# Kernel tuning notes

Hardware: AMD Instinct MI355X
Metric: run time of the kernel (lower is better)

## Reference

```python
import jax, jax.numpy as jnp
import numpy as np

N = 100000
E = 1600000
H = 128
G = 64  # num graphs


def setup_inputs() -> dict:
    key = jax.random.key(0)
    ks = jax.random.split(key, 20)
    s = 1.0 / np.sqrt(H)
    inp = {
        'x': jax.random.normal(ks[0], (N,), jnp.float32),
        'edge_index': jax.random.randint(ks[1], (2, E), 0, N, jnp.int32),
        'edge_attr': jax.random.normal(ks[2], (E, 1), jnp.float32),
        'batch': jnp.sort(jax.random.randint(ks[3], (N,), 0, G, jnp.int32)),
        # node/edge encoders (Linear(1, H))
        'ne_w': jax.random.normal(ks[4], (1, H), jnp.float32),
        'ne_b': jnp.zeros((H,), jnp.float32),
        'ee_w': jax.random.normal(ks[5], (1, H), jnp.float32),
        'ee_b': jnp.zeros((H,), jnp.float32),
        # conv1: internal edge lin (Linear(H,H)) + MLP (H->H->H)
        'lin1_w': jax.random.normal(ks[6], (H, H), jnp.float32) * s,
        'lin1_b': jnp.zeros((H,), jnp.float32),
        'w11': jax.random.normal(ks[7], (H, H), jnp.float32) * s,
        'b11': jnp.zeros((H,), jnp.float32),
        'w12': jax.random.normal(ks[8], (H, H), jnp.float32) * s,
        'b12': jnp.zeros((H,), jnp.float32),
        # conv2
        'lin2_w': jax.random.normal(ks[9], (H, H), jnp.float32) * s,
        'lin2_b': jnp.zeros((H,), jnp.float32),
        'w21': jax.random.normal(ks[10], (H, H), jnp.float32) * s,
        'b21': jnp.zeros((H,), jnp.float32),
        'w22': jax.random.normal(ks[11], (H, H), jnp.float32) * s,
        'b22': jnp.zeros((H,), jnp.float32),
    }
    return inp


def _gine(h, edge_index, e, lin_w, lin_b, w1, b1, w2, b2, eps=0.0):
    # message: ReLU(x_j + Lin(edge_attr)), aggregated (sum) at target nodes
    src, dst = edge_index[0], edge_index[1]
    m = jax.nn.relu(h[src] + e @ lin_w + lin_b)           # [E, H]
    agg = jax.ops.segment_sum(m, dst, num_segments=N)      # [N, H]
    z = (1.0 + eps) * h + agg
    return jax.nn.relu(z @ w1 + b1) @ w2 + b2


def reference(x, edge_index, edge_attr, batch, ne_w, ne_b, ee_w, ee_b,
              lin1_w, lin1_b, w11, b11, w12, b12,
              lin2_w, lin2_b, w21, b21, w22, b22):
    h = x.reshape(-1, 1) @ ne_w + ne_b                     # [N, H]
    e = edge_attr @ ee_w + ee_b                            # [E, H]
    h = jax.nn.relu(_gine(h, edge_index, e, lin1_w, lin1_b, w11, b11, w12, b12))
    h = jax.nn.relu(_gine(h, edge_index, e, lin2_w, lin2_b, w21, b21, w22, b22))
    # global mean pool per graph
    sums = jax.ops.segment_sum(h, batch, num_segments=G)   # [G, H]
    cnt = jax.ops.segment_sum(jnp.ones((N,), h.dtype), batch, num_segments=G)
    return sums / jnp.maximum(cnt, 1.0)[:, None]
```

## Files before the change

kernel.cpp:

```cpp
#include <hip/hip_runtime.h>

typedef unsigned short u16;
typedef unsigned int u32;
typedef __bf16 bfrag __attribute__((ext_vector_type(8)));
typedef float f32x4 __attribute__((ext_vector_type(4)));
typedef float f32x2 __attribute__((ext_vector_type(2)));

__device__ __forceinline__ u16 f2bf(float f) {
    u32 u = __float_as_uint(f);
    u32 r = (u + 0x7FFFu + ((u >> 16) & 1u)) >> 16;
    return (u16)r;
}
__device__ __forceinline__ float bf2f(u32 h) {
    return __uint_as_float(h << 16);
}

__global__ __launch_bounds__(1024) void prepack_bcount_kernel(
    const int* __restrict__ dst, int* __restrict__ bcnt, int* __restrict__ done,
    int* __restrict__ bstart, int* __restrict__ bcur, int E, int nb, int nbc,
    const float* __restrict__ w11, const float* __restrict__ w12,
    const float* __restrict__ w21, const float* __restrict__ w22,
    u16* __restrict__ hi, u16* __restrict__ lo,
    const float* __restrict__ ne_b, const float* __restrict__ ee_w, const float* __restrict__ ee_b,
    const float* __restrict__ lin1_w, const float* __restrict__ lin1_b,
    const float* __restrict__ lin2_w, const float* __restrict__ lin2_b,
    float* __restrict__ u1, float* __restrict__ C1, float* __restrict__ u2, float* __restrict__ C2)
{
    if (blockIdx.x >= (u32)nbc) {
        int pb = blockIdx.x - nbc;
        if (pb == 64) {
            int c = threadIdx.x;
            if (c < 128) {
                float s1 = 0.f, t1 = 0.f, s2 = 0.f, t2 = 0.f;
                for (int k = 0; k < 128; ++k) {
                    float w1 = lin1_w[k * 128 + c];
                    float w2 = lin2_w[k * 128 + c];
                    float ew = ee_w[k], eb = ee_b[k];
                    s1 = fmaf(ew, w1, s1); t1 = fmaf(eb, w1, t1);
                    s2 = fmaf(ew, w2, s2); t2 = fmaf(eb, w2, t2);
                }
                u1[c] = s1; C1[c] = t1 + lin1_b[c] + ne_b[c];
                u2[c] = s2; C2[c] = t2 + lin2_b[c];
            }
            return;
        }
        int which = pb >> 4;
        const float* w = (which == 0) ? w11 : (which == 1) ? w12 : (which == 2) ? w21 : w22;
        int o = (pb & 15) * 1024 + threadIdx.x;
        int j = o & 7;
        int lane = (o >> 3) & 63;
        int ct = (o >> 9) & 7;
        int ks = o >> 12;
        int k = ks * 32 + ((lane >> 4) * 8) + j;
        int c = ct * 16 + (lane & 15);
        float v = w[k * 128 + c];
        u16 h = f2bf(v);
        float vh = bf2f(h);
        u16 l = f2bf(v - vh);
        hi[which * 16384 + o] = h;
        lo[which * 16384 + o] = l;
        return;
    }

    __shared__ int h[256];
    __shared__ int is_last;
    if (threadIdx.x < 256) h[threadIdx.x] = 0;
    __syncthreads();
    int idx = blockIdx.x * 1024 + threadIdx.x;
    int e = idx * 4;
    if (e + 3 < E) {
        int4 d4 = ((const int4*)dst)[idx];
        atomicAdd(&h[d4.x >> 9], 1);
        atomicAdd(&h[d4.y >> 9], 1);
        atomicAdd(&h[d4.z >> 9], 1);
        atomicAdd(&h[d4.w >> 9], 1);
    } else {
        for (int k = e; k < E; ++k) atomicAdd(&h[dst[k] >> 9], 1);
    }
    __syncthreads();
    if (threadIdx.x < 256 && h[threadIdx.x]) atomicAdd(&bcnt[threadIdx.x], h[threadIdx.x]);
    __syncthreads();
    if (threadIdx.x == 0) {
        __threadfence();
        is_last = (atomicAdd(done, 1) == nbc - 1);
    }
    __syncthreads();
    if (!is_last) return;
    if (threadIdx.x < 256) h[threadIdx.x] = atomicAdd(&bcnt[threadIdx.x], 0);
    __syncthreads();
    __shared__ int excl[256];
    if (threadIdx.x < 64) {
        int l = threadIdx.x;
        int v0 = h[4 * l], v1 = h[4 * l + 1], v2 = h[4 * l + 2], v3 = h[4 * l + 3];
        int tot = v0 + v1 + v2 + v3;
        int run = tot;
#pragma unroll
        for (int off = 1; off < 64; off <<= 1) {
            int t = __shfl_up(run, off);
            if (l >= off) run += t;
        }
        int ex = run - tot;
        excl[4 * l] = ex;
        excl[4 * l + 1] = ex + v0;
        excl[4 * l + 2] = ex + v0 + v1;
        excl[4 * l + 3] = ex + v0 + v1 + v2;
    }
    __syncthreads();
    if (threadIdx.x < nb) {
        int ex = excl[threadIdx.x];
        bstart[threadIdx.x] = ex;
        bcur[threadIdx.x] = ex;
        if (threadIdx.x == nb - 1) bstart[nb] = ex + h[threadIdx.x];
    }
}

__global__ __launch_bounds__(1024) void bin_kernel(
    const int* __restrict__ src, const int* __restrict__ dst, const float* __restrict__ eattr,
    int* __restrict__ bucket_cursor,
    int2* __restrict__ binned, int E, int nb)
{
    __shared__ int hist[256];
    __shared__ int basel[256];
    __shared__ int gbase[256];
    __shared__ int2 stage[4096];
    __shared__ unsigned char sb[4096];
    const int tid = threadIdx.x;
    const int e0 = blockIdx.x * 4096;
    const int valid = min(4096, E - e0);

    if (tid < 256) hist[tid] = 0;
    __syncthreads();

    int d[4], s[4], a[4], rk[4];
    bool ok[4];
    const int eb = e0 + tid * 4;
    if (eb + 3 < E) {
        int4 d4 = *(const int4*)(dst + eb);
        int4 s4 = *(const int4*)(src + eb);
        int4 a4 = *(const int4*)((const int*)eattr + eb);
        d[0] = d4.x; d[1] = d4.y; d[2] = d4.z; d[3] = d4.w;
        s[0] = s4.x; s[1] = s4.y; s[2] = s4.z; s[3] = s4.w;
        a[0] = a4.x; a[1] = a4.y; a[2] = a4.z; a[3] = a4.w;
        ok[0] = ok[1] = ok[2] = ok[3] = true;
    } else {
#pragma unroll
        for (int k = 0; k < 4; ++k) {
            int e = eb + k;
            ok[k] = e < E;
            if (ok[k]) {
                d[k] = dst[e];
                s[k] = src[e];
                a[k] = __float_as_int(eattr[e]);
            }
        }
    }
#pragma unroll
    for (int k = 0; k < 4; ++k) {
        if (ok[k]) rk[k] = atomicAdd(&hist[d[k] >> 9], 1);
    }
    __syncthreads();
    if (tid < 64) {
        int l = tid;
        int v0 = hist[4 * l], v1 = hist[4 * l + 1], v2 = hist[4 * l + 2], v3 = hist[4 * l + 3];
        int tot = v0 + v1 + v2 + v3;
        int run = tot;
#pragma unroll
        for (int off = 1; off < 64; off <<= 1) {
            int t = __shfl_up(run, off);
            if (l >= off) run += t;
        }
        int ex = run - tot;
        basel[4 * l] = ex;
        basel[4 * l + 1] = ex + v0;
        basel[4 * l + 2] = ex + v0 + v1;
        basel[4 * l + 3] = ex + v0 + v1 + v2;
    }
    __syncthreads();
    if (tid < nb && hist[tid] > 0) gbase[tid] = atomicAdd(&bucket_cursor[tid], hist[tid]);
#pragma unroll
    for (int k = 0; k < 4; ++k) {
        if (ok[k]) {
            int b = d[k] >> 9;
            int pos = basel[b] + rk[k];
            stage[pos] = make_int2(s[k] | ((d[k] & 511) << 17), a[k]);
            sb[pos] = (unsigned char)b;
        }
    }
    __syncthreads();
    for (int i = tid; i < valid; i += 1024) {
        int b = (int)sb[i];
        binned[gbase[b] + (i - basel[b])] = stage[i];
    }
}

__global__ __launch_bounds__(1024) void fine_kernel(
    const int2* __restrict__ binned, const int* __restrict__ bstart,
    int* __restrict__ rowptr, int2* __restrict__ edges, int N, int nbuckets)
{
    __shared__ int hist[512];
    __shared__ int excl[512];
    const int tid = threadIdx.x;
    const int b = blockIdx.x;
    const int s0 = bstart[b], s1 = bstart[b + 1];
    if (tid < 512) hist[tid] = 0;
    __syncthreads();
    for (int i = s0 + tid; i < s1; i += 1024)
        atomicAdd(&hist[(binned[i].x >> 17) & 511], 1);
    __syncthreads();
    if (tid < 64) {
        int l = tid;
        int v[8], pre[8];
        int tot = 0;
#pragma unroll
        for (int k = 0; k < 8; ++k) { v[k] = hist[8 * l + k]; pre[k] = tot; tot += v[k]; }
        int run = tot;
#pragma unroll
        for (int off = 1; off < 64; off <<= 1) {
            int t = __shfl_up(run, off);
            if (l >= off) run += t;
        }
        int ex = run - tot;
#pragma unroll
        for (int k = 0; k < 8; ++k) excl[8 * l + k] = ex + pre[k];
    }
    __syncthreads();
    const int nbase = b << 9;
    if (tid < 512 && nbase + tid < N) rowptr[nbase + tid] = s0 + excl[tid];
    if (b == nbuckets - 1 && tid == 0) rowptr[N] = s1;
    __syncthreads();
    for (int i = s0 + tid; i < s1; i += 1024) {
        int2 ed = binned[i];
        int dlo = (ed.x >> 17) & 511;
        ed.x &= 0x1FFFF;
        int pos = atomicAdd(&excl[dlo], 1);
        edges[s0 + pos] = ed;
    }
}


__global__ __launch_bounds__(256) void pull1_kernel(
    const float* __restrict__ x,
    const int* __restrict__ rowptr, const int2* __restrict__ edges,
    const float* __restrict__ ne_w, const float* __restrict__ ne_b,
    const float* __restrict__ u1, const float* __restrict__ C1,
    u16* __restrict__ zb, int N)
{
    int lane = threadIdx.x & 63;
    int node = blockIdx.x * 4 + (threadIdx.x >> 6);
    if (node >= N) return;
    f32x2 A  = *(const f32x2*)(ne_w + 2 * lane);
    f32x2 Bv = *(const f32x2*)(u1   + 2 * lane);
    f32x2 Cv = *(const f32x2*)(C1   + 2 * lane);
    f32x2 nb = *(const f32x2*)(ne_b + 2 * lane);
    const f32x2 zero = {0.f, 0.f};
    int jb = rowptr[node], je = rowptr[node + 1];
    f32x2 acc = zero;
    int j = jb;
    for (; j + 8 <= je; j += 8) {
        float xs[8], av[8];
#pragma unroll
        for (int t = 0; t < 8; ++t) {
            int2 ep = edges[j + t];
            int s = __builtin_amdgcn_readfirstlane(ep.x);
            av[t] = __int_as_float(__builtin_amdgcn_readfirstlane(ep.y));
            xs[t] = x[s];
        }
#pragma unroll
        for (int t = 0; t < 8; ++t) {
            f32x2 m = __builtin_elementwise_fma((f32x2){xs[t], xs[t]}, A,
                        __builtin_elementwise_fma((f32x2){av[t], av[t]}, Bv, Cv));
            acc += __builtin_elementwise_max(m, zero);
        }
    }
    for (; j < je; ++j) {
        int2 ep = edges[j];
        int s = __builtin_amdgcn_readfirstlane(ep.x);
        float av = __int_as_float(__builtin_amdgcn_readfirstlane(ep.y));
        float xs = x[s];
        f32x2 m = __builtin_elementwise_fma((f32x2){xs, xs}, A,
                    __builtin_elementwise_fma((f32x2){av, av}, Bv, Cv));
        acc += __builtin_elementwise_max(m, zero);
    }
    float xn = x[node];
    f32x2 z = __builtin_elementwise_fma((f32x2){xn, xn}, A, nb) + acc;
    ((u32*)(zb + (long)node * 128))[lane] = (u32)f2bf(z.x) | ((u32)f2bf(z.y) << 16);
}

__global__ __launch_bounds__(256) void pull2_kernel(
    const u16* __restrict__ h1b,
    const int* __restrict__ rowptr, const int2* __restrict__ edges,
    const float* __restrict__ u2, const float* __restrict__ C2,
    u16* __restrict__ zb2, int N)
{
    int lane = threadIdx.x & 63;
    int node = blockIdx.x * 4 + (threadIdx.x >> 6);
    if (node >= N) return;
    f32x2 Bv = *(const f32x2*)(u2 + 2 * lane);
    f32x2 Cv = *(const f32x2*)(C2 + 2 * lane);
    const f32x2 zero = {0.f, 0.f};
    int jb = rowptr[node], je = rowptr[node + 1];
    f32x2 acc = zero;
    int j = jb;
    for (; j + 8 <= je; j += 8) {
        int sidx[8];
        float av[8];
        u32 hv[8];
#pragma unroll
        for (int t = 0; t < 8; ++t) {
            int2 ep = edges[j + t];
            sidx[t] = __builtin_amdgcn_readfirstlane(ep.x);
            av[t] = __int_as_float(__builtin_amdgcn_readfirstlane(ep.y));
        }
#pragma unroll
        for (int t = 0; t < 8; ++t)
            hv[t] = *(const u32*)(h1b + (long)sidx[t] * 128 + 2 * lane);
#pragma unroll
        for (int t = 0; t < 8; ++t) {
            f32x2 h = { __uint_as_float(hv[t] << 16), __uint_as_float(hv[t] & 0xFFFF0000u) };
            f32x2 m = h + __builtin_elementwise_fma((f32x2){av[t], av[t]}, Bv, Cv);
            acc += __builtin_elementwise_max(m, zero);
        }
    }
    for (; j < je; ++j) {
        int2 ep = edges[j];
        int s = __builtin_amdgcn_readfirstlane(ep.x);
        float av = __int_as_float(__builtin_amdgcn_readfirstlane(ep.y));
        u32 hv = *(const u32*)(h1b + (long)s * 128 + 2 * lane);
        f32x2 h = { __uint_as_float(hv << 16), __uint_as_float(hv & 0xFFFF0000u) };
        f32x2 m = h + __builtin_elementwise_fma((f32x2){av, av}, Bv, Cv);
        acc += __builtin_elementwise_max(m, zero);
    }
    u32 hn = *(const u32*)(h1b + (long)node * 128 + 2 * lane);
    f32x2 hnv = { __uint_as_float(hn << 16), __uint_as_float(hn & 0xFFFF0000u) };
    f32x2 z = hnv + acc;
    ((u32*)(zb2 + (long)node * 128))[lane] = (u32)f2bf(z.x) | ((u32)f2bf(z.y) << 16);
}

__global__ __launch_bounds__(256) void mlp_kernel(
    const u16* __restrict__ zb,
    const u16* __restrict__ w1hi, const u16* __restrict__ w1lo,
    const u16* __restrict__ w2hi, const u16* __restrict__ w2lo,
    const float* __restrict__ b1, const float* __restrict__ b2,
    u16* __restrict__ outb)
{
    __shared__ __align__(16) u16 tls[64][136];
    const int lane = threadIdx.x & 63;
    const int wv = threadIdx.x >> 6;
    const int m = lane & 15;
    const int q = lane >> 4;
    const int ko = q * 8;
    const long tile_row = (long)blockIdx.x * 64 + wv * 16;

    f32x4 acc[8];
#pragma unroll
    for (int ct = 0; ct < 8; ++ct) acc[ct] = (f32x4){0.f, 0.f, 0.f, 0.f};

#pragma unroll
    for (int ks = 0; ks < 4; ++ks) {
        bfrag a = *(const bfrag*)(zb + (tile_row + m) * 128 + ks * 32 + ko);
#pragma unroll
        for (int ct = 0; ct < 8; ++ct) {
            const int off = (((ks * 8 + ct) * 64) + lane) * 8;
            bfrag bh = *(const bfrag*)(w1hi + off);
            bfrag bl = *(const bfrag*)(w1lo + off);
            acc[ct] = __builtin_amdgcn_mfma_f32_16x16x32_bf16(a, bh, acc[ct], 0, 0, 0);
            acc[ct] = __builtin_amdgcn_mfma_f32_16x16x32_bf16(a, bl, acc[ct], 0, 0, 0);
        }
    }
#pragma unroll
    for (int ct = 0; ct < 8; ++ct) {
        float bv = b1[ct * 16 + m];
#pragma unroll
        for (int r = 0; r < 4; ++r) {
            float v = fmaxf(acc[ct][r] + bv, 0.f);
            tls[wv * 16 + q * 4 + r][ct * 16 + m] = f2bf(v);
        }
    }
    __syncthreads();

    f32x4 acc2[8];
#pragma unroll
    for (int ct = 0; ct < 8; ++ct) acc2[ct] = (f32x4){0.f, 0.f, 0.f, 0.f};

#pragma unroll
    for (int ks = 0; ks < 4; ++ks) {
        bfrag a = *(const bfrag*)(&tls[wv * 16 + m][ks * 32 + ko]);
#pragma unroll
        for (int ct = 0; ct < 8; ++ct) {
            const int off = (((ks * 8 + ct) * 64) + lane) * 8;
            bfrag bh = *(const bfrag*)(w2hi + off);
            bfrag bl = *(const bfrag*)(w2lo + off);
            acc2[ct] = __builtin_amdgcn_mfma_f32_16x16x32_bf16(a, bh, acc2[ct], 0, 0, 0);
            acc2[ct] = __builtin_amdgcn_mfma_f32_16x16x32_bf16(a, bl, acc2[ct], 0, 0, 0);
        }
    }
    __syncthreads();
#pragma unroll
    for (int ct = 0; ct < 8; ++ct) {
        float bv = b2[ct * 16 + m];
#pragma unroll
        for (int r = 0; r < 4; ++r) {
            float v = fmaxf(acc2[ct][r] + bv, 0.f);
            tls[wv * 16 + q * 4 + r][ct * 16 + m] = f2bf(v);
        }
    }
    __syncthreads();
    const long base_row = (long)blockIdx.x * 64;
#pragma unroll
    for (int it = 0; it < 4; ++it) {
        int chunk = threadIdx.x + it * 256;
        int row = chunk >> 4;
        int c8 = (chunk & 15) * 8;
        *(uint4*)(outb + (base_row + row) * 128 + c8) = *(const uint4*)(&tls[row][c8]);
    }
}

__global__ __launch_bounds__(256) void mlp_pool_kernel(
    const u16* __restrict__ zb,
    const u16* __restrict__ w1hi, const u16* __restrict__ w1lo,
    const u16* __restrict__ w2hi, const u16* __restrict__ w2lo,
    const float* __restrict__ b1, const float* __restrict__ b2,
    const int* __restrict__ batch, float* __restrict__ poolacc, int N)
{
    __shared__ __align__(16) u16 tls[64][136];
    __shared__ int bsh[64];
    const int lane = threadIdx.x & 63;
    const int wv = threadIdx.x >> 6;
    const int m = lane & 15;
    const int q = lane >> 4;
    const int ko = q * 8;
    const long tile_row = (long)blockIdx.x * 64 + wv * 16;
    const long base_row = (long)blockIdx.x * 64;

    if (threadIdx.x < 64) {
        long node = base_row + threadIdx.x;
        bsh[threadIdx.x] = (node < N) ? batch[node] : -1;
    }

    f32x4 acc[8];
#pragma unroll
    for (int ct = 0; ct < 8; ++ct) acc[ct] = (f32x4){0.f, 0.f, 0.f, 0.f};

#pragma unroll
    for (int ks = 0; ks < 4; ++ks) {
        bfrag a = *(const bfrag*)(zb + (tile_row + m) * 128 + ks * 32 + ko);
#pragma unroll
        for (int ct = 0; ct < 8; ++ct) {
            const int off = (((ks * 8 + ct) * 64) + lane) * 8;
            bfrag bh = *(const bfrag*)(w1hi + off);
            bfrag bl = *(const bfrag*)(w1lo + off);
            acc[ct] = __builtin_amdgcn_mfma_f32_16x16x32_bf16(a, bh, acc[ct], 0, 0, 0);
            acc[ct] = __builtin_amdgcn_mfma_f32_16x16x32_bf16(a, bl, acc[ct], 0, 0, 0);
        }
    }
#pragma unroll
    for (int ct = 0; ct < 8; ++ct) {
        float bv = b1[ct * 16 + m];
#pragma unroll
        for (int r = 0; r < 4; ++r) {
            float v = fmaxf(acc[ct][r] + bv, 0.f);
            tls[wv * 16 + q * 4 + r][ct * 16 + m] = f2bf(v);
        }
    }
    __syncthreads();

    f32x4 acc2[8];
#pragma unroll
    for (int ct = 0; ct < 8; ++ct) acc2[ct] = (f32x4){0.f, 0.f, 0.f, 0.f};

#pragma unroll
    for (int ks = 0; ks < 4; ++ks) {
        bfrag a = *(const bfrag*)(&tls[wv * 16 + m][ks * 32 + ko]);
#pragma unroll
        for (int ct = 0; ct < 8; ++ct) {
            const int off = (((ks * 8 + ct) * 64) + lane) * 8;
            bfrag bh = *(const bfrag*)(w2hi + off);
            bfrag bl = *(const bfrag*)(w2lo + off);
            acc2[ct] = __builtin_amdgcn_mfma_f32_16x16x32_bf16(a, bh, acc2[ct], 0, 0, 0);
            acc2[ct] = __builtin_amdgcn_mfma_f32_16x16x32_bf16(a, bl, acc2[ct], 0, 0, 0);
        }
    }
    __syncthreads();
#pragma unroll
    for (int ct = 0; ct < 8; ++ct) {
        float bv = b2[ct * 16 + m];
#pragma unroll
        for (int r = 0; r < 4; ++r) {
            float v = fmaxf(acc2[ct][r] + bv, 0.f);
            tls[wv * 16 + q * 4 + r][ct * 16 + m] = f2bf(v);
        }
    }
    __syncthreads();

    int c = threadIdx.x & 127;
    int half = threadIdx.x >> 7;
    int r0 = half * 32, r1 = r0 + 32;
    int cur = -1;
    float sum = 0.f;
    for (int r = r0; r < r1; ++r) {
        int g = bsh[r];
        if (g < 0) break;
        float v = bf2f((u32)tls[r][c]);
        if (g != cur) {
            if (cur >= 0) atomicAdd(&poolacc[cur * 128 + c], sum);
            sum = 0.f;
            cur = g;
        }
        sum += v;
    }
    if (cur >= 0) atomicAdd(&poolacc[cur * 128 + c], sum);
}

__global__ __launch_bounds__(128) void pool2_kernel(
    const float* __restrict__ acc, const int* __restrict__ batch,
    float* __restrict__ out, int n)
{
    int g = blockIdx.x;
    int c = threadIdx.x;
    int lo = 0, hi = n;
    while (lo < hi) { int mid = (lo + hi) >> 1; if (batch[mid] < g) lo = mid + 1; else hi = mid; }
    int s = lo;
    lo = s; hi = n;
    while (lo < hi) { int mid = (lo + hi) >> 1; if (batch[mid] < g + 1) lo = mid + 1; else hi = mid; }
    int cnt = lo - s;
    out[g * 128 + c] = acc[g * 128 + c] / (float)(cnt > 0 ? cnt : 1);
}

extern "C" void kernel_launch(void* const* d_in, const int* in_sizes, int n_in,
                              void* d_out, int out_size, void* d_ws, size_t ws_size,
                              hipStream_t stream)
{
    const float* x      = (const float*)d_in[0];
    const int*   ei     = (const int*)d_in[1];
    const float* eattr  = (const float*)d_in[2];
    const int*   batch  = (const int*)d_in[3];
    const float* ne_w   = (const float*)d_in[4];
    const float* ne_b   = (const float*)d_in[5];
    const float* ee_w   = (const float*)d_in[6];
    const float* ee_b   = (const float*)d_in[7];
    const float* lin1_w = (const float*)d_in[8];
    const float* lin1_b = (const float*)d_in[9];
    const float* w11    = (const float*)d_in[10];
    const float* b11    = (const float*)d_in[11];
    const float* w12    = (const float*)d_in[12];
    const float* b12    = (const float*)d_in[13];
    const float* lin2_w = (const float*)d_in[14];
    const float* lin2_b = (const float*)d_in[15];
    const float* w21    = (const float*)d_in[16];
    const float* b21    = (const float*)d_in[17];
    const float* w22    = (const float*)d_in[18];
    const float* b22    = (const float*)d_in[19];

    const int N = in_sizes[0];
    const int E = in_sizes[2];
    const int G = out_size / 128;
    const int Npad = ((N + 63) / 64) * 64;
    const int nb = (N + 511) >> 9;
    const int nbc = (E + 4095) / 4096;
    const int* esrc = ei;
    const int* edst = ei + E;

    char* p = (char*)d_ws;
    auto alloc = [&](size_t bytes) -> void* {
        void* r = (void*)p;
        p += (bytes + 255) & ~(size_t)255;
        return r;
    };
    float* u1 = (float*)alloc(128 * 4);
    float* C1 = (float*)alloc(128 * 4);
    float* u2 = (float*)alloc(128 * 4);
    float* C2 = (float*)alloc(128 * 4);
    int* bcnt   = (int*)alloc(1024);
    int* done   = (int*)alloc(256);
    float* poolacc = (float*)alloc((size_t)G * 128 * 4);
    int* bstart = (int*)alloc(((size_t)nb + 1) * 4);
    int* bcur   = (int*)alloc((size_t)nb * 4);
    int* rowptr = (int*)alloc(((size_t)N + 1) * 4);
    int2* edges = (int2*)alloc((size_t)E * 8);
    int2* binned = (int2*)alloc((size_t)E * 8);
    u16* whi = (u16*)alloc((size_t)4 * 16384 * 2);
    u16* wlo = (u16*)alloc((size_t)4 * 16384 * 2);
    u16* bufA = (u16*)alloc((size_t)Npad * 128 * 2);
    u16* bufB = (u16*)alloc((size_t)Npad * 128 * 2);

    size_t zbytes = (size_t)((char*)poolacc + (size_t)G * 128 * 4 - (char*)bcnt);
    hipMemsetAsync(bcnt, 0, zbytes, stream);

    prepack_bcount_kernel<<<nbc + 65, 1024, 0, stream>>>(
        edst, bcnt, done, bstart, bcur, E, nb, nbc,
        w11, w12, w21, w22, whi, wlo,
        ne_b, ee_w, ee_b, lin1_w, lin1_b, lin2_w, lin2_b, u1, C1, u2, C2);

    bin_kernel<<<nbc, 1024, 0, stream>>>(esrc, edst, eattr, bcur, binned, E, nb);
    fine_kernel<<<nb, 1024, 0, stream>>>(binned, bstart, rowptr, edges, N, nb);

    pull1_kernel<<<(N + 3) / 4, 256, 0, stream>>>(x, rowptr, edges, ne_w, ne_b, u1, C1,
                                                  bufA, N);
    mlp_kernel<<<Npad / 64, 256, 0, stream>>>(bufA, whi, wlo, whi + 16384, wlo + 16384,
                                              b11, b12, bufB);
    pull2_kernel<<<(N + 3) / 4, 256, 0, stream>>>(bufB, rowptr, edges, u2, C2, bufA, N);
    mlp_pool_kernel<<<Npad / 64, 256, 0, stream>>>(bufA, whi + 32768, wlo + 32768,
                                                   whi + 49152, wlo + 49152, b21, b22,
                                                   batch, poolacc, N);

    pool2_kernel<<<G, 128, 0, stream>>>(poolacc, batch, (float*)d_out, N);
}
```

Before: 361.9 us.

## Process four consecutive CSR nodes per wavefront with 32-edge batched gathers

Both pull kernels now give each wavefront four consecutive destination nodes and walk their combined edge range as one stream, flushing the accumulator at row boundaries. Edge records are loaded 32 at a time with one coalesced vector load and broadcast with readlane, and the next batch is prefetched while the current one is accumulated. The goal is to cut per-node overhead and tail loops, since nodes average about 16 edges, and to keep more gathers in flight. The cost is extra boundary-compare branches per edge and more register pressure from the 32-wide unrolled arrays, which the occupancy hint in launch bounds may fight against.

```diff
diff --git a/kernel.cpp b/kernel.cpp
--- a/kernel.cpp
+++ b/kernel.cpp
@@ -238,102 +238,205 @@
 }
 
 
-__global__ __launch_bounds__(256) void pull1_kernel(
+__global__ __launch_bounds__(256, 8) void pull1_kernel(
     const float* __restrict__ x,
     const int* __restrict__ rowptr, const int2* __restrict__ edges,
     const float* __restrict__ ne_w, const float* __restrict__ ne_b,
     const float* __restrict__ u1, const float* __restrict__ C1,
     u16* __restrict__ zb, int N)
 {
-    int lane = threadIdx.x & 63;
-    int node = blockIdx.x * 4 + (threadIdx.x >> 6);
-    if (node >= N) return;
-    f32x2 A  = *(const f32x2*)(ne_w + 2 * lane);
-    f32x2 Bv = *(const f32x2*)(u1   + 2 * lane);
-    f32x2 Cv = *(const f32x2*)(C1   + 2 * lane);
-    f32x2 nb = *(const f32x2*)(ne_b + 2 * lane);
+    const int lane = threadIdx.x & 63;
+    const int quad = blockIdx.x * 4 + (threadIdx.x >> 6);
+    const int n0 = quad * 4;
+    if (n0 >= N) return;
+    f32x2 A   = *(const f32x2*)(ne_w + 2 * lane);
+    f32x2 Bv  = *(const f32x2*)(u1   + 2 * lane);
+    f32x2 Cv  = *(const f32x2*)(C1   + 2 * lane);
+    f32x2 nbv = *(const f32x2*)(ne_b + 2 * lane);
     const f32x2 zero = {0.f, 0.f};
-    int jb = rowptr[node], je = rowptr[node + 1];
+    const int r1  = rowptr[min(n0 + 1, N)];
+    const int r2  = rowptr[min(n0 + 2, N)];
+    const int r3  = rowptr[min(n0 + 3, N)];
+    const int end = rowptr[min(n0 + 4, N)];
+    int e = rowptr[n0];
+    float xn0 = x[n0];
+    float xn1 = (n0 + 1 < N) ? x[n0 + 1] : 0.f;
+    float xn2 = (n0 + 2 < N) ? x[n0 + 2] : 0.f;
+    float xn3 = (n0 + 3 < N) ? x[n0 + 3] : 0.f;
     f32x2 acc = zero;
-    int j = jb;
-    for (; j + 8 <= je; j += 8) {
+    int done = 0;
+
+    auto flush = [&](int c, float xn) {
+        int node = n0 + c;
+        if (node < N) {
+            f32x2 z = __builtin_elementwise_fma((f32x2){xn, xn}, A, nbv) + acc;
+            ((u32*)(zb + (long)node * 128))[lane] = (u32)f2bf(z.x) | ((u32)f2bf(z.y) << 16);
+        }
+        acc = zero;
+        done = c + 1;
+    };
+    auto bcheck = [&](int ei) {
+        if (done < 1 && ei == r1) flush(0, xn0);
+        if (done < 2 && ei == r2) flush(1, xn1);
+        if (done < 3 && ei == r3) flush(2, xn2);
+    };
+    auto emit = [&](float xs, float av) {
+        f32x2 m = __builtin_elementwise_fma((f32x2){xs, xs}, A,
+                    __builtin_elementwise_fma((f32x2){av, av}, Bv, Cv));
+        acc += __builtin_elementwise_max(m, zero);
+    };
+
+    if (e + 32 <= end) {
+        int2 ep = edges[e + (lane & 31)];
+        while (true) {
+            float xs[32], av[32];
+#pragma unroll
+            for (int t = 0; t < 32; ++t) {
+                int s = __builtin_amdgcn_readlane(ep.x, t);
+                av[t] = __int_as_float(__builtin_amdgcn_readlane(ep.y, t));
+                xs[t] = x[s];
+            }
+            int enext = e + 32;
+            bool more = (enext + 32 <= end);
+            if (more) ep = edges[enext + (lane & 31)];
+#pragma unroll
+            for (int t = 0; t < 32; ++t) {
+                bcheck(e + t);
+                emit(xs[t], av[t]);
+            }
+            e = enext;
+            if (!more) break;
+        }
+    }
+    while (e + 8 <= end) {
+        int2 ep8 = edges[e + (lane & 7)];
         float xs[8], av[8];
 #pragma unroll
         for (int t = 0; t < 8; ++t) {
-            int2 ep = edges[j + t];
-            int s = __builtin_amdgcn_readfirstlane(ep.x);
-            av[t] = __int_as_float(__builtin_amdgcn_readfirstlane(ep.y));
+            int s = __builtin_amdgcn_readlane(ep8.x, t);
+            av[t] = __int_as_float(__builtin_amdgcn_readlane(ep8.y, t));
             xs[t] = x[s];
         }
 #pragma unroll
         for (int t = 0; t < 8; ++t) {
-            f32x2 m = __builtin_elementwise_fma((f32x2){xs[t], xs[t]}, A,
-                        __builtin_elementwise_fma((f32x2){av[t], av[t]}, Bv, Cv));
-            acc += __builtin_elementwise_max(m, zero);
-        }
-    }
-    for (; j < je; ++j) {
-        int2 ep = edges[j];
+            bcheck(e + t);
+            emit(xs[t], av[t]);
+        }
+        e += 8;
+    }
+    for (; e < end; ++e) {
+        int2 ep = edges[e];
         int s = __builtin_amdgcn_readfirstlane(ep.x);
         float av = __int_as_float(__builtin_amdgcn_readfirstlane(ep.y));
         float xs = x[s];
-        f32x2 m = __builtin_elementwise_fma((f32x2){xs, xs}, A,
-                    __builtin_elementwise_fma((f32x2){av, av}, Bv, Cv));
-        acc += __builtin_elementwise_max(m, zero);
-    }
-    float xn = x[node];
-    f32x2 z = __builtin_elementwise_fma((f32x2){xn, xn}, A, nb) + acc;
-    ((u32*)(zb + (long)node * 128))[lane] = (u32)f2bf(z.x) | ((u32)f2bf(z.y) << 16);
-}
-
-__global__ __launch_bounds__(256) void pull2_kernel(
+        bcheck(e);
+        emit(xs, av);
+    }
+    if (done < 1) flush(0, xn0);
+    if (done < 2) flush(1, xn1);
+    if (done < 3) flush(2, xn2);
+    flush(3, xn3);
+}
+
+__global__ __launch_bounds__(256, 8) void pull2_kernel(
     const u16* __restrict__ h1b,
     const int* __restrict__ rowptr, const int2* __restrict__ edges,
     const float* __restrict__ u2, const float* __restrict__ C2,
     u16* __restrict__ zb2, int N)
 {
-    int lane = threadIdx.x & 63;
-    int node = blockIdx.x * 4 + (threadIdx.x >> 6);
-    if (node >= N) return;
-    f32x2 Bv = *(const f32x2*)(u2 + 2 * lane);
-    f32x2 Cv = *(const f32x2*)(C2 + 2 * lane);
+    const int lane = threadIdx.x & 63;
+    const int lane2 = 2 * lane;
+    const int quad = blockIdx.x * 4 + (threadIdx.x >> 6);
+    const int n0 = quad * 4;
+    if (n0 >= N) return;
+    f32x2 Bv = *(const f32x2*)(u2 + lane2);
+    f32x2 Cv = *(const f32x2*)(C2 + lane2);
     const f32x2 zero = {0.f, 0.f};
-    int jb = rowptr[node], je = rowptr[node + 1];
+    const int r1  = rowptr[min(n0 + 1, N)];
+    const int r2  = rowptr[min(n0 + 2, N)];
+    const int r3  = rowptr[min(n0 + 3, N)];
+    const int end = rowptr[min(n0 + 4, N)];
+    int e = rowptr[n0];
+    u32 hn0 = *(const u32*)(h1b + (long)n0 * 128 + lane2);
+    u32 hn1 = (n0 + 1 < N) ? *(const u32*)(h1b + (long)(n0 + 1) * 128 + lane2) : 0u;
+    u32 hn2 = (n0 + 2 < N) ? *(const u32*)(h1b + (long)(n0 + 2) * 128 + lane2) : 0u;
+    u32 hn3 = (n0 + 3 < N) ? *(const u32*)(h1b + (long)(n0 + 3) * 128 + lane2) : 0u;
     f32x2 acc = zero;
-    int j = jb;
-    for (; j + 8 <= je; j += 8) {
-        int sidx[8];
-        float av[8];
-        u32 hv[8];
-#pragma unroll
-        for (int t = 0; t < 8; ++t) {
-            int2 ep = edges[j + t];
-            sidx[t] = __builtin_amdgcn_readfirstlane(ep.x);
-            av[t] = __int_as_float(__builtin_amdgcn_readfirstlane(ep.y));
-        }
-#pragma unroll
-        for (int t = 0; t < 8; ++t)
-            hv[t] = *(const u32*)(h1b + (long)sidx[t] * 128 + 2 * lane);
-#pragma unroll
-        for (int t = 0; t < 8; ++t) {
-            f32x2 h = { __uint_as_float(hv[t] << 16), __uint_as_float(hv[t] & 0xFFFF0000u) };
-            f32x2 m = h + __builtin_elementwise_fma((f32x2){av[t], av[t]}, Bv, Cv);
-            acc += __builtin_elementwise_max(m, zero);
-        }
-    }
-    for (; j < je; ++j) {
-        int2 ep = edges[j];
-        int s = __builtin_amdgcn_readfirstlane(ep.x);
-        float av = __int_as_float(__builtin_amdgcn_readfirstlane(ep.y));
-        u32 hv = *(const u32*)(h1b + (long)s * 128 + 2 * lane);
+    int done = 0;
+
+    auto flush = [&](int c, u32 hn) {
+        int node = n0 + c;
+        if (node < N) {
+            f32x2 h = { __uint_as_float(hn << 16), __uint_as_float(hn & 0xFFFF0000u) };
+            f32x2 z = h + acc;
+            ((u32*)(zb2 + (long)node * 128))[lane] = (u32)f2bf(z.x) | ((u32)f2bf(z.y) << 16);
+        }
+        acc = zero;
+        done = c + 1;
+    };
+    auto bcheck = [&](int ei) {
+        if (done < 1 && ei == r1) flush(0, hn0);
+        if (done < 2 && ei == r2) flush(1, hn1);
+        if (done < 3 && ei == r3) flush(2, hn2);
+    };
+    auto emit = [&](u32 hv, float av) {
         f32x2 h = { __uint_as_float(hv << 16), __uint_as_float(hv & 0xFFFF0000u) };
         f32x2 m = h + __builtin_elementwise_fma((f32x2){av, av}, Bv, Cv);
         acc += __builtin_elementwise_max(m, zero);
-    }
-    u32 hn = *(const u32*)(h1b + (long)node * 128 + 2 * lane);
-    f32x2 hnv = { __uint_as_float(hn << 16), __uint_as_float(hn & 0xFFFF0000u) };
-    f32x2 z = hnv + acc;
-    ((u32*)(zb2 + (long)node * 128))[lane] = (u32)f2bf(z.x) | ((u32)f2bf(z.y) << 16);
+    };
+
+    if (e + 32 <= end) {
+        int2 ep = edges[e + (lane & 31)];
+        while (true) {
+            u32 hv[32];
+            float av[32];
+#pragma unroll
+            for (int t = 0; t < 32; ++t) {
+                int s = __builtin_amdgcn_readlane(ep.x, t);
+                av[t] = __int_as_float(__builtin_amdgcn_readlane(ep.y, t));
+                hv[t] = *(const u32*)(h1b + (long)s * 128 + lane2);
+            }
+            int enext = e + 32;
+            bool more = (enext + 32 <= end);
+            if (more) ep = edges[enext + (lane & 31)];
+#pragma unroll
+            for (int t = 0; t < 32; ++t) {
+                bcheck(e + t);
+                emit(hv[t], av[t]);
+            }
+            e = enext;
+            if (!more) break;
+        }
+    }
+    while (e + 8 <= end) {
+        int2 ep8 = edges[e + (lane & 7)];
+        u32 hv[8];
+        float av[8];
+#pragma unroll
+        for (int t = 0; t < 8; ++t) {
+            int s = __builtin_amdgcn_readlane(ep8.x, t);
+            av[t] = __int_as_float(__builtin_amdgcn_readlane(ep8.y, t));
+            hv[t] = *(const u32*)(h1b + (long)s * 128 + lane2);
+        }
+#pragma unroll
+        for (int t = 0; t < 8; ++t) {
+            bcheck(e + t);
+            emit(hv[t], av[t]);
+        }
+        e += 8;
+    }
+    for (; e < end; ++e) {
+        int2 ep = edges[e];
+        int s = __builtin_amdgcn_readfirstlane(ep.x);
+        float av = __int_as_float(__builtin_amdgcn_readfirstlane(ep.y));
+        u32 hv = *(const u32*)(h1b + (long)s * 128 + lane2);
+        bcheck(e);
+        emit(hv, av);
+    }
+    if (done < 1) flush(0, hn0);
+    if (done < 2) flush(1, hn1);
+    if (done < 3) flush(2, hn2);
+    flush(3, hn3);
 }
 
 __global__ __launch_bounds__(256) void mlp_kernel(
@@ -594,11 +697,11 @@
     bin_kernel<<<nbc, 1024, 0, stream>>>(esrc, edst, eattr, bcur, binned, E, nb);
     fine_kernel<<<nb, 1024, 0, stream>>>(binned, bstart, rowptr, edges, N, nb);
 
-    pull1_kernel<<<(N + 3) / 4, 256, 0, stream>>>(x, rowptr, edges, ne_w, ne_b, u1, C1,
-                                                  bufA, N);
+    pull1_kernel<<<(N + 15) / 16, 256, 0, stream>>>(x, rowptr, edges, ne_w, ne_b, u1, C1,
+                                                    bufA, N);
     mlp_kernel<<<Npad / 64, 256, 0, stream>>>(bufA, whi, wlo, whi + 16384, wlo + 16384,
                                               b11, b12, bufB);
-    pull2_kernel<<<(N + 3) / 4, 256, 0, stream>>>(bufB, rowptr, edges, u2, C2, bufA, N);
+    pull2_kernel<<<(N + 15) / 16, 256, 0, stream>>>(bufB, rowptr, edges, u2, C2, bufA, N);
     mlp_pool_kernel<<<Npad / 64, 256, 0, stream>>>(bufA, whi + 32768, wlo + 32768,
                                                    whi + 49152, wlo + 49152, b21, b22,
                                                    batch, poolacc, N);
```

New measurement: 433.3 us. 19.7% more time.
